# Kernel optimization log

Hardware: AMD Instinct MI355X
Metric: run time of the kernel (lower is better)

Reference implementation:

```python
import jax, jax.numpy as jnp
import numpy as np

# Module/problem constants (match init_kwargs & input_specs)
B, D, H, W = 2, 96, 96, 96
CIN, COUT, K = 16, 32, 3
N = 200000  # number of active (sparse) voxels


def setup_inputs() -> dict:
    key = jax.random.key(0)
    kf, kw, kb = jax.random.split(key, 3)
    # unique valid voxel coordinates -> deterministic scatter semantics
    rng = np.random.default_rng(0)
    lin = rng.choice(B * D * H * W, size=N, replace=False)
    b, z, y, x = np.unravel_index(lin, (B, D, H, W))
    indices = jnp.asarray(np.stack([b, z, y, x], axis=1).astype(np.int32))  # [N,4]
    features = jax.random.normal(kf, (N, CIN), dtype=jnp.float32)
    fan_in = CIN * K ** 3
    conv_w = jax.random.normal(kw, (COUT, CIN, K, K, K), dtype=jnp.float32) / np.sqrt(fan_in)
    conv_b = jax.random.normal(kb, (COUT,), dtype=jnp.float32) * 0.01
    return {"features": features, "indices": indices, "conv_w": conv_w, "conv_b": conv_b}


def reference(features, indices, conv_w, conv_b):
    """DenseFallbackConv3d.forward on a SparseConvTensor, stride=1 path.

    1) scatter sparse features into dense grid [B,CIN,D,H,W]
    2) dense Conv3d (k=3, pad=1, stride=1) + bias
    3) gather per-point output features at the same voxel indices -> [N,COUT]
    """
    b = indices[:, 0]
    z = indices[:, 1]
    y = indices[:, 2]
    x = indices[:, 3]
    # scatter: equivalent of grid[b, :, z, y, x] = features
    grid = jnp.zeros((B, CIN, D, H, W), dtype=features.dtype).at[b, :, z, y, x].set(features)
    out = jax.lax.conv_general_dilated(
        grid, conv_w,
        window_strides=(1, 1, 1),
        padding=((1, 1), (1, 1), (1, 1)),
        dimension_numbers=("NCDHW", "OIDHW", "NCDHW"),
    )
    out = out + conv_b[None, :, None, None, None]
    # gather: out_dense[b, :, z, y, x] for every active voxel -> [N, COUT]
    return out[b, :, z, y, x]
```

## Files before the change

kernel.cpp:

```cpp
#include <hip/hip_runtime.h>

#define BB   2
#define DD   96
#define HH   96
#define WW   96
#define CINC 16
#define COUTC 32
#define KVOL 27
#define GRID_VOX (BB*DD*HH*WW)
#define NW (KVOL*CINC*COUTC)
#define VPT 8
#define CVB (256*VPT)

typedef _Float16 half8 __attribute__((ext_vector_type(8)));
typedef float    floatx16 __attribute__((ext_vector_type(16)));

__global__ __launch_bounds__(256) void setup_kernel(
        const int* __restrict__ idx, int* __restrict__ g,
        const float* __restrict__ w, _Float16* __restrict__ wH,
        int* __restrict__ counter, int n, int scatter_blocks) {
    if ((int)blockIdx.x < scatter_blocks) {
        int i = blockIdx.x * 256 + threadIdx.x;
        if (i >= n) return;
        int4 v = ((const int4*)idx)[i];
        int lin = ((v.x * DD + v.y) * HH + v.z) * WW + v.w;
        g[lin] = i;
    } else {
        int t = ((int)blockIdx.x - scatter_blocks) * 256 + threadIdx.x;
        if (t == 0) counter[0] = 0;
        if (t >= NW) return;
        int ci = t & (CINC - 1);
        int co = (t >> 4) & (COUTC - 1);
        int kk = t >> 9;
        wH[t] = (_Float16)w[(co * CINC + ci) * KVOL + kk];
    }
}

__global__ __launch_bounds__(256) void compact_kernel(
        const int* __restrict__ idx, const float* __restrict__ feat,
        int* __restrict__ g, _Float16* __restrict__ featH,
        int* __restrict__ pc, int* __restrict__ perm,
        int* __restrict__ counter, int n) {
    __shared__ int s_wsum[4];
    __shared__ int s_wbase[4];
    __shared__ int s_base;
    const int t = threadIdx.x;
    const int lane = t & 63;
    const int wv = t >> 6;
    const int base = blockIdx.x * CVB + t * VPT;

    int4 a0 = ((const int4*)(g + base))[0];
    int4 a1 = ((const int4*)(g + base))[1];
    int vals[VPT] = {a0.x, a0.y, a0.z, a0.w, a1.x, a1.y, a1.z, a1.w};
    int pid[VPT], pck[VPT];
    int cnt = 0;
#pragma unroll
    for (int q = 0; q < VPT; ++q) {
        int p = vals[q];
        bool ok = ((unsigned)p < (unsigned)n);
        int pk = 0;
        if (ok) {
            int4 c = ((const int4*)idx)[p];
            int lin = ((c.x * DD + c.y) * HH + c.z) * WW + c.w;
            ok = (lin == base + q);
            pk = (c.x << 21) | (c.y << 14) | (c.z << 7) | c.w;
        }
        pid[q] = ok ? p : -1;
        pck[q] = pk;
        cnt += ok ? 1 : 0;
    }

    int incl = cnt;
#pragma unroll
    for (int d = 1; d < 64; d <<= 1) {
        int v = __shfl_up(incl, d);
        if (lane >= d) incl += v;
    }
    if (lane == 63) s_wsum[wv] = incl;
    __syncthreads();
    if (t == 0) {
        int t0 = s_wsum[0], t1 = s_wsum[1], t2 = s_wsum[2], t3 = s_wsum[3];
        s_wbase[0] = 0; s_wbase[1] = t0; s_wbase[2] = t0 + t1;
        s_wbase[3] = t0 + t1 + t2;
        s_base = atomicAdd(counter, t0 + t1 + t2 + t3);
    }
    __syncthreads();
    int o = s_base + s_wbase[wv] + incl - cnt;

#pragma unroll
    for (int q = 0; q < VPT; ++q) {
        int tag = n;
        int p = pid[q];
        if (p >= 0) {
            pc[o] = pck[q];
            perm[o] = p;
            const float4* src = (const float4*)(feat + (size_t)p * CINC);
            float4 f0 = src[0], f1 = src[1], f2 = src[2], f3 = src[3];
            half8 h0, h1;
            h0[0]=(_Float16)f0.x; h0[1]=(_Float16)f0.y; h0[2]=(_Float16)f0.z; h0[3]=(_Float16)f0.w;
            h0[4]=(_Float16)f1.x; h0[5]=(_Float16)f1.y; h0[6]=(_Float16)f1.z; h0[7]=(_Float16)f1.w;
            h1[0]=(_Float16)f2.x; h1[1]=(_Float16)f2.y; h1[2]=(_Float16)f2.z; h1[3]=(_Float16)f2.w;
            h1[4]=(_Float16)f3.x; h1[5]=(_Float16)f3.y; h1[6]=(_Float16)f3.z; h1[7]=(_Float16)f3.w;
            half8* dst = (half8*)(featH + (size_t)o * CINC);
            dst[0] = h0; dst[1] = h1;
            tag = o;
            ++o;
        }
        g[base + q] = tag;
    }
    if (blockIdx.x == 0 && t == 0) {
        half8* zr = (half8*)(featH + (size_t)n * CINC);
        half8 hz = {};
        zr[0] = hz; zr[1] = hz;
    }
}

__global__ __launch_bounds__(256, 4) void conv_mfma_kernel(
        const _Float16* __restrict__ featH, const int* __restrict__ pc,
        const int* __restrict__ perm, const _Float16* __restrict__ wH,
        const float* __restrict__ bias, const int* __restrict__ g,
        float* __restrict__ out, int n) {
    __shared__ _Float16 sW[KVOL * 64 * 8];
    const int lane = threadIdx.x & 63;
    const int wave = threadIdx.x >> 6;
    const int m    = lane & 31;
    const int hf   = lane >> 5;

    for (int u = threadIdx.x; u < KVOL * 64; u += 256) {
        int kk = u >> 6, r = u & 63;
        int mm = r & 31, h = r >> 5;
        half8 v = *(const half8*)(wH + kk * (COUTC * CINC) + mm * CINC + h * 8);
        *(half8*)(&sW[(size_t)u * 8]) = v;
    }
    __syncthreads();

    const int j0 = (blockIdx.x * 4 + wave) * 32;
    if (j0 >= n) return;
    const int j = j0 + m;

    const int p = pc[j];
    const int x = p & 127, y = (p >> 7) & 127, z = (p >> 14) & 127, b = p >> 21;
    const int base = ((b * DD + z) * HH + y) * WW + x;
    const int pm = perm[j];

    int nid[KVOL];
#pragma unroll
    for (int kk = 0; kk < KVOL; ++kk) {
        const int dz = kk / 9 - 1, dy = (kk / 3) % 3 - 1, dx = kk % 3 - 1;
        int nz = z + dz, ny = y + dy, nx = x + dx;
        bool inb = ((unsigned)nz < DD) & ((unsigned)ny < HH) & ((unsigned)nx < WW);
        int addr = inb ? base + (dz * HH + dy) * WW + dx : 0;
        int v = g[addr];
        nid[kk] = inb ? v : n;
    }

    float bval = bias[m];
    floatx16 acc;
#pragma unroll
    for (int i = 0; i < 16; ++i) acc[i] = bval;

#pragma unroll
    for (int gq = 0; gq < 3; ++gq) {
        half8 av[9];
#pragma unroll
        for (int q = 0; q < 9; ++q)
            av[q] = *(const half8*)(featH + (size_t)nid[gq * 9 + q] * CINC + hf * 8);
#pragma unroll
        for (int q = 0; q < 9; ++q) {
            const int kk = gq * 9 + q;
            half8 bf = *(const half8*)(&sW[((size_t)kk * 64 + hf * 32 + m) * 8]);
            acc = __builtin_amdgcn_mfma_f32_32x32x16_f16(av[q], bf, acc, 0, 0, 0);
        }
    }

#pragma unroll
    for (int i = 0; i < 16; ++i) {
        int r = (i & 3) + 8 * (i >> 2) + 4 * hf;
        int row = __shfl(pm, r);
        out[(size_t)row * COUTC + m] = acc[i];
    }
}

extern "C" void kernel_launch(void* const* d_in, const int* in_sizes, int n_in,
                              void* d_out, int out_size, void* d_ws, size_t ws_size,
                              hipStream_t stream) {
    const float* feat  = (const float*)d_in[0];
    const int*   idx   = (const int*)d_in[1];
    const float* convw = (const float*)d_in[2];
    const float* convb = (const float*)d_in[3];
    float* out = (float*)d_out;

    const int n = in_sizes[1] / 4;

    char* ws = (char*)d_ws;
    int*      g       = (int*)ws;
    int*      counter = (int*)(ws + GRID_VOX * 4);
    int*      pc      = (int*)(ws + GRID_VOX * 4 + 256);
    int*      perm    = pc + n;
    _Float16* featH   = (_Float16*)(perm + n);
    _Float16* wH      = featH + (size_t)(n + 1) * CINC;

    const int sb = (n + 255) / 256;
    const int rb = (NW + 255) / 256;
    setup_kernel<<<sb + rb, 256, 0, stream>>>(idx, g, convw, wH, counter, n, sb);
    compact_kernel<<<GRID_VOX / CVB, 256, 0, stream>>>(
        idx, feat, g, featH, pc, perm, counter, n);

    const int waves = (n + 31) / 32;
    conv_mfma_kernel<<<(waves + 3) / 4, 256, 0, stream>>>(
        featH, pc, perm, wH, convb, g, out, n);
}
```

Baseline: 122.5 us.

## Clear voxel grid with memset and convert features in original order

The voxel grid is now cleared to -1 with a memset before scattering, so the compaction pass no longer re-reads each candidate point's coordinates to reject stale grid entries. It also no longer rewrites the grid with compacted ids. Instead it rebuilds packed coordinates from the linear voxel index. Feature conversion to fp16 moves into the setup kernel and is indexed by original point id, and the conv kernel uses the grid values directly as feature rows. This removes random idx reads and a full grid rewrite from compaction. In exchange it adds a full-grid memset pass, and neighbour feature gathers in the conv kernel lose the spatial locality the compacted ordering gave them.

```diff
diff --git a/kernel.cpp b/kernel.cpp
--- a/kernel.cpp
+++ b/kernel.cpp
@@ -17,17 +17,36 @@
 
 __global__ __launch_bounds__(256) void setup_kernel(
         const int* __restrict__ idx, int* __restrict__ g,
+        const float* __restrict__ feat, _Float16* __restrict__ featH,
         const float* __restrict__ w, _Float16* __restrict__ wH,
-        int* __restrict__ counter, int n, int scatter_blocks) {
-    if ((int)blockIdx.x < scatter_blocks) {
-        int i = blockIdx.x * 256 + threadIdx.x;
+        int* __restrict__ counter, int n, int sb, int fb) {
+    const int bid = blockIdx.x;
+    if (bid < sb) {
+        int i = bid * 256 + threadIdx.x;
         if (i >= n) return;
         int4 v = ((const int4*)idx)[i];
         int lin = ((v.x * DD + v.y) * HH + v.z) * WW + v.w;
         g[lin] = i;
+    } else if (bid < sb + fb) {
+        int i = (bid - sb) * 256 + threadIdx.x;
+        if (i >= n) return;
+        const float4* src = (const float4*)(feat + (size_t)i * CINC);
+        float4 f0 = src[0], f1 = src[1], f2 = src[2], f3 = src[3];
+        half8 h0, h1;
+        h0[0]=(_Float16)f0.x; h0[1]=(_Float16)f0.y; h0[2]=(_Float16)f0.z; h0[3]=(_Float16)f0.w;
+        h0[4]=(_Float16)f1.x; h0[5]=(_Float16)f1.y; h0[6]=(_Float16)f1.z; h0[7]=(_Float16)f1.w;
+        h1[0]=(_Float16)f2.x; h1[1]=(_Float16)f2.y; h1[2]=(_Float16)f2.z; h1[3]=(_Float16)f2.w;
+        h1[4]=(_Float16)f3.x; h1[5]=(_Float16)f3.y; h1[6]=(_Float16)f3.z; h1[7]=(_Float16)f3.w;
+        half8* dst = (half8*)(featH + (size_t)i * CINC);
+        dst[0] = h0; dst[1] = h1;
     } else {
-        int t = ((int)blockIdx.x - scatter_blocks) * 256 + threadIdx.x;
-        if (t == 0) counter[0] = 0;
+        int t = (bid - sb - fb) * 256 + threadIdx.x;
+        if (t == 0) {
+            counter[0] = 0;
+            half8 hz = {};
+            half8* zr = (half8*)(featH + (size_t)n * CINC);
+            zr[0] = hz; zr[1] = hz;
+        }
         if (t >= NW) return;
         int ci = t & (CINC - 1);
         int co = (t >> 4) & (COUTC - 1);
@@ -37,10 +56,8 @@
 }
 
 __global__ __launch_bounds__(256) void compact_kernel(
-        const int* __restrict__ idx, const float* __restrict__ feat,
-        int* __restrict__ g, _Float16* __restrict__ featH,
-        int* __restrict__ pc, int* __restrict__ perm,
-        int* __restrict__ counter, int n) {
+        const int* __restrict__ g, int* __restrict__ pc,
+        int* __restrict__ perm, int* __restrict__ counter, int n) {
     __shared__ int s_wsum[4];
     __shared__ int s_wbase[4];
     __shared__ int s_base;
@@ -52,21 +69,13 @@
     int4 a0 = ((const int4*)(g + base))[0];
     int4 a1 = ((const int4*)(g + base))[1];
     int vals[VPT] = {a0.x, a0.y, a0.z, a0.w, a1.x, a1.y, a1.z, a1.w};
-    int pid[VPT], pck[VPT];
+    int pid[VPT];
     int cnt = 0;
 #pragma unroll
     for (int q = 0; q < VPT; ++q) {
         int p = vals[q];
         bool ok = ((unsigned)p < (unsigned)n);
-        int pk = 0;
-        if (ok) {
-            int4 c = ((const int4*)idx)[p];
-            int lin = ((c.x * DD + c.y) * HH + c.z) * WW + c.w;
-            ok = (lin == base + q);
-            pk = (c.x << 21) | (c.y << 14) | (c.z << 7) | c.w;
-        }
         pid[q] = ok ? p : -1;
-        pck[q] = pk;
         cnt += ok ? 1 : 0;
     }
 
@@ -89,29 +98,19 @@
 
 #pragma unroll
     for (int q = 0; q < VPT; ++q) {
-        int tag = n;
         int p = pid[q];
         if (p >= 0) {
-            pc[o] = pck[q];
+            int v = base + q;
+            int b = (v >= DD * HH * WW) ? 1 : 0;
+            int rem = v - b * (DD * HH * WW);
+            int z = rem / (HH * WW);
+            int r2 = rem - z * (HH * WW);
+            int y = r2 / WW;
+            int x = r2 - y * WW;
+            pc[o] = (b << 21) | (z << 14) | (y << 7) | x;
             perm[o] = p;
-            const float4* src = (const float4*)(feat + (size_t)p * CINC);
-            float4 f0 = src[0], f1 = src[1], f2 = src[2], f3 = src[3];
-            half8 h0, h1;
-            h0[0]=(_Float16)f0.x; h0[1]=(_Float16)f0.y; h0[2]=(_Float16)f0.z; h0[3]=(_Float16)f0.w;
-            h0[4]=(_Float16)f1.x; h0[5]=(_Float16)f1.y; h0[6]=(_Float16)f1.z; h0[7]=(_Float16)f1.w;
-            h1[0]=(_Float16)f2.x; h1[1]=(_Float16)f2.y; h1[2]=(_Float16)f2.z; h1[3]=(_Float16)f2.w;
-            h1[4]=(_Float16)f3.x; h1[5]=(_Float16)f3.y; h1[6]=(_Float16)f3.z; h1[7]=(_Float16)f3.w;
-            half8* dst = (half8*)(featH + (size_t)o * CINC);
-            dst[0] = h0; dst[1] = h1;
-            tag = o;
             ++o;
         }
-        g[base + q] = tag;
-    }
-    if (blockIdx.x == 0 && t == 0) {
-        half8* zr = (half8*)(featH + (size_t)n * CINC);
-        half8 hz = {};
-        zr[0] = hz; zr[1] = hz;
     }
 }
 
@@ -151,7 +150,8 @@
         bool inb = ((unsigned)nz < DD) & ((unsigned)ny < HH) & ((unsigned)nx < WW);
         int addr = inb ? base + (dz * HH + dy) * WW + dx : 0;
         int v = g[addr];
-        nid[kk] = inb ? v : n;
+        bool ok = inb & ((unsigned)v < (unsigned)n);
+        nid[kk] = ok ? v : n;
     }
 
     float bval = bias[m];
@@ -201,10 +201,13 @@
     _Float16* wH      = featH + (size_t)(n + 1) * CINC;
 
     const int sb = (n + 255) / 256;
+    const int fb = (n + 255) / 256;
     const int rb = (NW + 255) / 256;
-    setup_kernel<<<sb + rb, 256, 0, stream>>>(idx, g, convw, wH, counter, n, sb);
-    compact_kernel<<<GRID_VOX / CVB, 256, 0, stream>>>(
-        idx, feat, g, featH, pc, perm, counter, n);
+
+    hipMemsetAsync(g, 0xFF, (size_t)GRID_VOX * 4, stream);
+    setup_kernel<<<sb + fb + rb, 256, 0, stream>>>(
+        idx, g, feat, featH, convw, wH, counter, n, sb, fb);
+    compact_kernel<<<GRID_VOX / CVB, 256, 0, stream>>>(g, pc, perm, counter, n);
 
     const int waves = (n + 31) / 32;
     conv_mfma_kernel<<<(waves + 3) / 4, 256, 0, stream>>>(
```

Result: faster. 115.3 us (-5.8%).
